# Optimization experiments

Measured on AMD Instinct MI355X. Metric: run time of the kernel, lower is better.

## Reference

```python
import jax, jax.numpy as jnp
import numpy as np

D_MODEL = 512
HEADS = 8
MAX_LEN = 2048


def setup_inputs() -> dict:
    key = jax.random.key(0)
    ks = jax.random.split(key, 8)
    b, t, e, h = 2, 2048, D_MODEL, HEADS
    s = e // h
    x = jax.random.normal(ks[0], (b, t, e), dtype=jnp.float32)
    mask = jax.random.randint(ks[1], (b, t), 0, 2).astype(jnp.int32)
    Wq = jax.random.normal(ks[2], (s, s), dtype=jnp.float32) / np.sqrt(s)
    Wk = jax.random.normal(ks[3], (s, s), dtype=jnp.float32) / np.sqrt(s)
    Wv = jax.random.normal(ks[4], (s, s), dtype=jnp.float32) / np.sqrt(s)
    Er = jax.random.normal(ks[5], (h, MAX_LEN, s), dtype=jnp.float32)
    Wo = jax.random.normal(ks[6], (e, e), dtype=jnp.float32) / np.sqrt(e)
    bo = jnp.zeros((e,), dtype=jnp.float32)
    return {"x": x, "mask": mask, "heads": h, "Wq": Wq, "Wk": Wk, "Wv": Wv,
            "Er": Er, "Wo": Wo, "bo": bo}


def reference(x, mask, heads, Wq, Wk, Wv, Er, Wo, bo):
    b, t, e = x.shape
    h = heads
    s = e // h
    x4 = x.reshape(b, t, h, s)
    # per-head shared linear projections (nn.Linear applies x @ W^T), then (b,h,t,s)
    q = jnp.einsum('bthi,oi->bhto', x4, Wq)
    k = jnp.einsum('bthi,oi->bhto', x4, Wk)
    v = jnp.einsum('bthi,oi->bhto', x4, Wv)
    # relative position scores: QEr computed on UNSCALED queries (as in source)
    Er_t = Er[:, Er.shape[1] - t:, :]                  # (h, t, s)
    qe = jnp.einsum('bhts,hls->bhtl', q, Er_t)          # (b, h, t, t)
    idx = jnp.arange(t)
    # _mask_positions: zero where col < t-1-row (flipped upper triangle)
    keep = (idx[None, :] >= (t - 1 - idx[:, None]))
    qe = jnp.where(keep[None, None], qe, 0.0)
    # _skew: pad one column on the left, reshape (t, t+1)->(t+1, t), drop first row
    padded = jnp.pad(qe, ((0, 0), (0, 0), (0, 0), (1, 0)))
    srel = padded.reshape(b, h, t + 1, t)[:, :, 1:, :]  # (b, h, t, t)
    scale = e ** (-0.25)
    scores = jnp.einsum('bhts,bhls->bhtl', q * scale, k * scale) + srel
    neg = jnp.float32(-1e9)
    causal = idx[None, :] > idx[:, None]                # future positions
    scores = jnp.where(causal[None, None], neg, scores)
    # padding mask zeroes entire query rows
    scores = jnp.where(mask[:, None, :, None] == 0, neg, scores)
    probs = jax.nn.softmax(scores, axis=-1)
    out = jnp.einsum('bhtl,bhls->bths', probs, v)       # (b, h, t, s)
    out = out.transpose(0, 2, 1, 3).reshape(b, t, e)
    return out @ Wo.T + bo
```

## Files before the change

### kernel.cpp

```cpp
#include <hip/hip_runtime.h>


#define B_ 2
#define T_ 2048
#define E_ 512
#define H_ 8
#define SCALE2 0.044194173824159216f

typedef __attribute__((ext_vector_type(8))) short bf16x8;
typedef __attribute__((ext_vector_type(4))) float f32x4;

#define MFMA(a,b,c) __builtin_amdgcn_mfma_f32_16x16x32_bf16((a),(b),(c),0,0,0)

__device__ __forceinline__ unsigned short f2bf(float f){
  unsigned u = __builtin_bit_cast(unsigned, f);
  u += 0x7fffu + ((u >> 16) & 1u);
  return (unsigned short)(u >> 16);
}
__device__ __forceinline__ float bf2f(unsigned short h){
  unsigned u = ((unsigned)h) << 16;
  return __builtin_bit_cast(float, u);
}

__global__ __launch_bounds__(256) void prep_qkv(
    const float* __restrict__ x,
    const float* __restrict__ Wq, const float* __restrict__ Wk, const float* __restrict__ Wv,
    unsigned short* __restrict__ qh, unsigned short* __restrict__ ql,
    unsigned short* __restrict__ kb, unsigned short* __restrict__ vb)
{
  int wid = blockIdx.x*4 + (threadIdx.x>>6);
  int o   = threadIdx.x & 63;
  int bh  = wid & 15;
  int rest = wid >> 4;
  int chunk = rest & 127;
  int m = rest >> 7;
  const float* W = (m==0) ? Wq : (m==1) ? Wk : Wv;
  float4 wv[16];
  #pragma unroll
  for (int j=0;j<16;++j) wv[j] = reinterpret_cast<const float4*>(W)[o*16+j];
  if (m==1){
    #pragma unroll
    for (int j=0;j<16;++j){ wv[j].x*=SCALE2; wv[j].y*=SCALE2; wv[j].z*=SCALE2; wv[j].w*=SCALE2; }
  }
  int b = bh>>3, h = bh&7;
  unsigned short* out0 = (m==0) ? qh : (m==1) ? kb : vb;
  for (int tl=0; tl<16; ++tl){
    int t = chunk*16 + tl;
    const float4* xr = reinterpret_cast<const float4*>(x + ((size_t)(b*T_ + t))*E_ + h*64);
    float a0=0.f,a1=0.f,a2=0.f,a3=0.f;
    #pragma unroll
    for (int j=0;j<16;++j){
      float4 xv = xr[j];
      a0 += xv.x*wv[j].x; a1 += xv.y*wv[j].y; a2 += xv.z*wv[j].z; a3 += xv.w*wv[j].w;
    }
    float acc = (a0+a1)+(a2+a3);
    size_t oi = ((size_t)bh*T_ + t)*64 + o;
    if (m==0){
      unsigned short hq = f2bf(acc);
      out0[oi] = hq;
      ql[oi] = f2bf(acc - bf2f(hq));
    } else {
      out0[oi] = f2bf(acc);
    }
  }
}

__global__ void prep_er(const float* __restrict__ Er,
                        unsigned short* __restrict__ eh, unsigned short* __restrict__ el)
{
  int i = (blockIdx.x*blockDim.x + threadIdx.x)*4;
  float4 v = *reinterpret_cast<const float4*>(Er + i);
  unsigned short h0=f2bf(v.x), h1=f2bf(v.y), h2=f2bf(v.z), h3=f2bf(v.w);
  *reinterpret_cast<ushort4*>(&eh[i]) = make_ushort4(h0,h1,h2,h3);
  *reinterpret_cast<ushort4*>(&el[i]) = make_ushort4(
      f2bf(v.x-bf2f(h0)), f2bf(v.y-bf2f(h1)), f2bf(v.z-bf2f(h2)), f2bf(v.w-bf2f(h3)));
}

__global__ void prep_wo(const float* __restrict__ Wo, unsigned short* __restrict__ wob){
  int i = (blockIdx.x*blockDim.x + threadIdx.x)*4;
  float4 v = *reinterpret_cast<const float4*>(Wo + i);
  *reinterpret_cast<ushort4*>(&wob[i]) = make_ushort4(f2bf(v.x),f2bf(v.y),f2bf(v.z),f2bf(v.w));
}

__global__ __launch_bounds__(256) void vsum1(const unsigned short* __restrict__ vb,
                                             float* __restrict__ vpart)
{
  __shared__ float red[4][64];
  int bh = blockIdx.x >> 3, ch = blockIdx.x & 7;
  int s = threadIdx.x & 63, sub = threadIdx.x >> 6;
  const unsigned short* p = vb + ((size_t)bh*T_ + ch*256 + sub*64)*64 + s;
  float acc = 0.f;
  #pragma unroll 8
  for (int t=0;t<64;++t) acc += bf2f(p[(size_t)t*64]);
  red[sub][s] = acc;
  __syncthreads();
  if (sub==0) vpart[(size_t)(bh*8+ch)*64 + s] = red[0][s]+red[1][s]+red[2][s]+red[3][s];
}
__global__ void vsum2(const float* __restrict__ vpart, float* __restrict__ vsum){
  int bh = blockIdx.x, s = threadIdx.x;
  float a = 0.f;
  #pragma unroll
  for (int c=0;c<8;++c) a += vpart[(size_t)(bh*8+c)*64 + s];
  vsum[bh*64+s] = a;
}

__global__ __launch_bounds__(256,2) void attn(
  const unsigned short* __restrict__ qh, const unsigned short* __restrict__ ql,
  const unsigned short* __restrict__ kb, const unsigned short* __restrict__ vb,
  const unsigned short* __restrict__ eh, const unsigned short* __restrict__ el,
  const int* __restrict__ mask, const float* __restrict__ vsum,
  unsigned short* __restrict__ ao)
{
  __shared__ float QEs[4][128][20];
  __shared__ unsigned short Ps[4][16][72];
  __shared__ unsigned short Vt[64][72];

  const int tid = threadIdx.x;
  const int w = tid >> 6, lane = tid & 63, g = lane >> 4, q15 = lane & 15;
  const int bid = blockIdx.x;
  const int bh = bid & 15;
  const int u = bid >> 4;
  const int rt = (u < 16) ? (2*u) : (63 - 2*u);
  const int i0 = rt * 64;
  const int b = bh >> 3, h = bh & 7;

  const size_t qoff = ((size_t)bh*T_ + i0 + 16*w + q15)*64 + 8*g;
  const bf16x8 qa00 = *(const bf16x8*)(qh + qoff);
  const bf16x8 qa01 = *(const bf16x8*)(qh + qoff + 32);
  const bf16x8 qa10 = *(const bf16x8*)(ql + qoff);
  const bf16x8 qa11 = *(const bf16x8*)(ql + qoff + 32);

  f32x4 oacc[4];
  float mrun[4], lrun[4];
  const f32x4 fz = {0.f,0.f,0.f,0.f};
  #pragma unroll
  for (int n=0;n<4;++n) oacc[n] = fz;
  #pragma unroll
  for (int p=0;p<4;++p){ mrun[p] = -1e30f; lrun[p] = 0.f; }

  const int ntiles = i0/64 + 1;
  const int lstart0 = (T_-64) - i0;
  for (int tI=0; tI<ntiles; ++tI){
    const int j0 = tI*64;
    const int lstart = lstart0 + j0;
    bf16x8 kf[4][2];
    #pragma unroll
    for (int n=0;n<4;++n){
      const unsigned short* kp = kb + ((size_t)bh*T_ + j0 + 16*n + q15)*64 + 8*g;
      kf[n][0] = *(const bf16x8*)kp;
      kf[n][1] = *(const bf16x8*)(kp+32);
    }
    const int key = tid & 63, sh = tid >> 6;
    bf16x8 vv0 = *(const bf16x8*)(vb + ((size_t)bh*T_ + j0 + key)*64 + 8*sh);
    bf16x8 vv1 = *(const bf16x8*)(vb + ((size_t)bh*T_ + j0 + key)*64 + 8*sh + 32);
    __syncthreads();
    #pragma unroll
    for (int jj=0;jj<8;++jj) Vt[8*sh+jj][key]    = (unsigned short)vv0[jj];
    #pragma unroll
    for (int jj=0;jj<8;++jj) Vt[8*sh+32+jj][key] = (unsigned short)vv1[jj];

    const int nhalf = (tI==0) ? 2 : 1;
    for (int half=0; half<nhalf; ++half){
      const int lb = (tI==0) ? (lstart + 64*half) : (lstart + 64);
      bf16x8 pe[4][4];
      #pragma unroll
      for (int g2=0; g2<4; ++g2){
        int ln = lb + 16*g2 + q15;
        int l = (ln > T_-1) ? (T_-1) : ln;
        const unsigned short* ep  = eh + ((size_t)h*T_ + l)*64 + 8*g;
        const unsigned short* ep2 = el + ((size_t)h*T_ + l)*64 + 8*g;
        pe[g2][0] = *(const bf16x8*)ep;
        pe[g2][1] = *(const bf16x8*)(ep+32);
        pe[g2][2] = *(const bf16x8*)ep2;
        pe[g2][3] = *(const bf16x8*)(ep2+32);
      }
      #pragma unroll
      for (int g2=0; g2<4; ++g2){
        int slot = (lb + 16*g2 + q15) & 127;
        f32x4 qe = {0.f,0.f,0.f,0.f};
        qe = MFMA(qa00, pe[g2][0], qe); qe = MFMA(qa01, pe[g2][1], qe);
        qe = MFMA(qa10, pe[g2][0], qe); qe = MFMA(qa11, pe[g2][1], qe);
        qe = MFMA(qa00, pe[g2][2], qe); qe = MFMA(qa01, pe[g2][3], qe);
        *(f32x4*)&QEs[w][slot][4*g] = qe;
      }
    }
    f32x4 sacc[4];
    #pragma unroll
    for (int n=0;n<4;++n){
      f32x4 s = fz;
      s = MFMA(qa00, kf[n][0], s); s = MFMA(qa01, kf[n][1], s);
      sacc[n] = s;
    }
    const bool lastT = (tI == ntiles-1);
    float pv[4][4];
    float tmax[4] = {-1e30f,-1e30f,-1e30f,-1e30f};
    #pragma unroll
    for (int n=0;n<4;++n){
      #pragma unroll
      for (int p=0;p<4;++p){
        int r = 16*w + 4*g + p;
        int c = 16*n + q15;
        int slot = (lstart + 63 - r + c) & 127;
        float s = sacc[n][p] + QEs[w][slot][4*g + p];
        if (lastT && c > r) s = -1e30f;
        pv[n][p] = s;
        tmax[p] = fmaxf(tmax[p], s);
      }
    }
    #pragma unroll
    for (int p=0;p<4;++p){
      float m = tmax[p];
      m = fmaxf(m, __shfl_xor(m,1)); m = fmaxf(m, __shfl_xor(m,2));
      m = fmaxf(m, __shfl_xor(m,4)); m = fmaxf(m, __shfl_xor(m,8));
      float mn = fmaxf(mrun[p], m);
      float al = __expf(mrun[p] - mn);
      mrun[p] = mn;
      lrun[p] *= al;
      oacc[0][p]*=al; oacc[1][p]*=al; oacc[2][p]*=al; oacc[3][p]*=al;
      float sum = 0.f;
      #pragma unroll
      for (int n=0;n<4;++n){
        float e = __expf(pv[n][p] - mn);
        pv[n][p] = e;
        sum += e;
      }
      sum += __shfl_xor(sum,1); sum += __shfl_xor(sum,2);
      sum += __shfl_xor(sum,4); sum += __shfl_xor(sum,8);
      lrun[p] += sum;
      #pragma unroll
      for (int n=0;n<4;++n) Ps[w][4*g+p][16*n+q15] = f2bf(pv[n][p]);
    }
    __syncthreads();
    bf16x8 pa0 = *(const bf16x8*)&Ps[w][q15][8*g];
    bf16x8 pa1 = *(const bf16x8*)&Ps[w][q15][8*g+32];
    #pragma unroll
    for (int ns=0; ns<4; ++ns){
      bf16x8 v0 = *(const bf16x8*)&Vt[16*ns+q15][8*g];
      bf16x8 v1 = *(const bf16x8*)&Vt[16*ns+q15][8*g+32];
      oacc[ns] = MFMA(pa0, v0, oacc[ns]);
      oacc[ns] = MFMA(pa1, v1, oacc[ns]);
    }
  }
  #pragma unroll
  for (int p=0;p<4;++p){
    int r = i0 + 16*w + 4*g + p;
    int mk = mask[b*T_ + r];
    float inv = 1.f / lrun[p];
    int rr = h*256 + (r >> 3);
    int cb2 = (r & 7)*64;
    #pragma unroll
    for (int n=0;n<4;++n){
      int sc = 16*n + q15;
      float val = mk ? oacc[n][p]*inv : vsum[bh*64+sc]*(1.f/2048.f);
      ao[((size_t)(b*T_ + rr))*E_ + cb2 + sc] = f2bf(val);
    }
  }
}

__global__ __launch_bounds__(256) void outproj(
  const unsigned short* __restrict__ ao, const unsigned short* __restrict__ wob,
  const float* __restrict__ bo, float* __restrict__ out)
{
  int tid = threadIdx.x;
  int w = tid>>6, lane = tid&63, g = lane>>4, q15 = lane&15;
  int nb = blockIdx.x & 7, rb = blockIdx.x >> 3;
  size_t row = (size_t)rb*64 + 16*w + q15;
  const unsigned short* ap = ao + row*E_ + 8*g;
  const f32x4 fz = {0.f,0.f,0.f,0.f};
  f32x4 acc[4];
  #pragma unroll
  for (int n=0;n<4;++n) acc[n] = fz;
  #pragma unroll 4
  for (int kk=0; kk<16; ++kk){
    bf16x8 a = *(const bf16x8*)(ap + 32*kk);
    #pragma unroll
    for (int n=0;n<4;++n){
      bf16x8 bfr = *(const bf16x8*)(wob + ((size_t)(nb*64 + 16*n + q15))*E_ + 32*kk + 8*g);
      acc[n] = MFMA(a, bfr, acc[n]);
    }
  }
  #pragma unroll
  for (int n=0;n<4;++n){
    int col = nb*64 + 16*n + q15;
    float bv = bo[col];
    #pragma unroll
    for (int p=0;p<4;++p){
      size_t rr = (size_t)rb*64 + 16*w + 4*g + p;
      out[rr*E_ + col] = acc[n][p] + bv;
    }
  }
}

extern "C" void kernel_launch(void* const* d_in, const int* in_sizes, int n_in,
                              void* d_out, int out_size, void* d_ws, size_t ws_size,
                              hipStream_t stream)
{
  int ix=-1, ier=-1, iwo=-1, ibo=-1, c4[4], nc=0;
  for (int i=0;i<n_in;++i){
    switch(in_sizes[i]){
      case 2097152: ix  = i; break;
      case 1048576: ier = i; break;
      case 262144:  iwo = i; break;
      case 512:     ibo = i; break;
      case 4096:    if (nc<4) c4[nc++] = i; break;
      default: break;
    }
  }
  if (ix<0||ier<0||iwo<0||ibo<0||nc!=4){ ix=0;c4[0]=1;c4[1]=3;c4[2]=4;c4[3]=5;ier=6;iwo=7;ibo=8; }
  const float* x  = (const float*)d_in[ix];
  const int* mask = (const int*)d_in[c4[0]];
  const float* Wq = (const float*)d_in[c4[1]];
  const float* Wk = (const float*)d_in[c4[2]];
  const float* Wv = (const float*)d_in[c4[3]];
  const float* Er = (const float*)d_in[ier];
  const float* Wo = (const float*)d_in[iwo];
  const float* bo = (const float*)d_in[ibo];
  float* out = (float*)d_out;

  char* ws = (char*)d_ws;
  unsigned short* qh  = (unsigned short*)(ws + 0);
  unsigned short* ql  = (unsigned short*)(ws + 4194304);
  unsigned short* kb  = (unsigned short*)(ws + 8388608);
  unsigned short* vb  = (unsigned short*)(ws + 12582912);
  unsigned short* eh  = (unsigned short*)(ws + 16777216);
  unsigned short* el  = (unsigned short*)(ws + 18874368);
  unsigned short* wob = (unsigned short*)(ws + 20971520);
  unsigned short* ao  = (unsigned short*)(ws + 21495808);
  float* vsum  = (float*)(ws + 25690112);
  float* vpart = (float*)(ws + 25694208);

  hipLaunchKernelGGL(prep_qkv, dim3(1536), dim3(256), 0, stream, x, Wq, Wk, Wv, qh, ql, kb, vb);
  hipLaunchKernelGGL(prep_er,  dim3(1024), dim3(256), 0, stream, Er, eh, el);
  hipLaunchKernelGGL(prep_wo,  dim3(256),  dim3(256), 0, stream, Wo, wob);
  hipLaunchKernelGGL(vsum1,    dim3(128),  dim3(256), 0, stream, vb, vpart);
  hipLaunchKernelGGL(vsum2,    dim3(16),   dim3(64),  0, stream, vpart, vsum);
  hipLaunchKernelGGL(attn,     dim3(512),  dim3(256), 0, stream, qh, ql, kb, vb, eh, el, mask, vsum, ao);
  hipLaunchKernelGGL(outproj,  dim3(512),  dim3(256), 0, stream, ao, wob, bo, out);
}
```

Baseline: 250.1 us.

## Split long causal attention rows across two blocks with flash-decoding style merge

Query row tiles 16-31 now have their key range split into two halves processed by separate blocks. Each block writes its unnormalized output, running max and sum to a partial buffer, and a new merge kernel combines them with log-sum-exp rescaling and applies the padding mask. This is meant to balance work across more blocks (768 instead of 512) and shorten the critical path. The cost is an extra kernel launch and partial-buffer traffic. Separately, prep_qkv is given twice as many blocks, each handling 8 timesteps instead of 16.

```diff
diff --git a/kernel.cpp b/kernel.cpp
--- a/kernel.cpp
+++ b/kernel.cpp
@@ -32,8 +32,8 @@
   int o   = threadIdx.x & 63;
   int bh  = wid & 15;
   int rest = wid >> 4;
-  int chunk = rest & 127;
-  int m = rest >> 7;
+  int chunk = rest & 255;
+  int m = rest >> 8;
   const float* W = (m==0) ? Wq : (m==1) ? Wk : Wv;
   float4 wv[16];
   #pragma unroll
@@ -44,8 +44,8 @@
   }
   int b = bh>>3, h = bh&7;
   unsigned short* out0 = (m==0) ? qh : (m==1) ? kb : vb;
-  for (int tl=0; tl<16; ++tl){
-    int t = chunk*16 + tl;
+  for (int tl=0; tl<8; ++tl){
+    int t = chunk*8 + tl;
     const float4* xr = reinterpret_cast<const float4*>(x + ((size_t)(b*T_ + t))*E_ + h*64);
     float a0=0.f,a1=0.f,a2=0.f,a3=0.f;
     #pragma unroll
@@ -108,8 +108,7 @@
   const unsigned short* __restrict__ qh, const unsigned short* __restrict__ ql,
   const unsigned short* __restrict__ kb, const unsigned short* __restrict__ vb,
   const unsigned short* __restrict__ eh, const unsigned short* __restrict__ el,
-  const int* __restrict__ mask, const float* __restrict__ vsum,
-  unsigned short* __restrict__ ao)
+  float* __restrict__ part)
 {
   __shared__ float QEs[4][128][20];
   __shared__ unsigned short Ps[4][16][72];
@@ -119,10 +118,19 @@
   const int w = tid >> 6, lane = tid & 63, g = lane >> 4, q15 = lane & 15;
   const int bid = blockIdx.x;
   const int bh = bid & 15;
-  const int u = bid >> 4;
-  const int rt = (u < 16) ? (2*u) : (63 - 2*u);
+  const int unit = bid >> 4;
+  int rt, ts, te, half;
+  if (unit < 16){ rt = unit; ts = 0; te = rt+1; half = 0; }
+  else {
+    int j = unit - 16;
+    rt = 16 + (j >> 1);
+    half = j & 1;
+    int nt = rt + 1;
+    int nh = (nt + 1) >> 1;
+    if (half == 0){ ts = 0; te = nh; } else { ts = nh; te = nt; }
+  }
   const int i0 = rt * 64;
-  const int b = bh >> 3, h = bh & 7;
+  const int h = bh & 7;
 
   const size_t qoff = ((size_t)bh*T_ + i0 + 16*w + q15)*64 + 8*g;
   const bf16x8 qa00 = *(const bf16x8*)(qh + qoff);
@@ -138,9 +146,8 @@
   #pragma unroll
   for (int p=0;p<4;++p){ mrun[p] = -1e30f; lrun[p] = 0.f; }
 
-  const int ntiles = i0/64 + 1;
   const int lstart0 = (T_-64) - i0;
-  for (int tI=0; tI<ntiles; ++tI){
+  for (int tI=ts; tI<te; ++tI){
     const int j0 = tI*64;
     const int lstart = lstart0 + j0;
     bf16x8 kf[4][2];
@@ -159,9 +166,9 @@
     #pragma unroll
     for (int jj=0;jj<8;++jj) Vt[8*sh+32+jj][key] = (unsigned short)vv1[jj];
 
-    const int nhalf = (tI==0) ? 2 : 1;
-    for (int half=0; half<nhalf; ++half){
-      const int lb = (tI==0) ? (lstart + 64*half) : (lstart + 64);
+    const int nhalf = (tI==ts) ? 2 : 1;
+    for (int hf=0; hf<nhalf; ++hf){
+      const int lb = (tI==ts) ? (lstart + 64*hf) : (lstart + 64);
       bf16x8 pe[4][4];
       #pragma unroll
       for (int g2=0; g2<4; ++g2){
@@ -191,7 +198,7 @@
       s = MFMA(qa00, kf[n][0], s); s = MFMA(qa01, kf[n][1], s);
       sacc[n] = s;
     }
-    const bool lastT = (tI == ntiles-1);
+    const bool lastT = (j0 == i0);
     float pv[4][4];
     float tmax[4] = {-1e30f,-1e30f,-1e30f,-1e30f};
     #pragma unroll
@@ -244,17 +251,38 @@
   #pragma unroll
   for (int p=0;p<4;++p){
     int r = i0 + 16*w + 4*g + p;
-    int mk = mask[b*T_ + r];
-    float inv = 1.f / lrun[p];
-    int rr = h*256 + (r >> 3);
-    int cb2 = (r & 7)*64;
-    #pragma unroll
-    for (int n=0;n<4;++n){
-      int sc = 16*n + q15;
-      float val = mk ? oacc[n][p]*inv : vsum[bh*64+sc]*(1.f/2048.f);
-      ao[((size_t)(b*T_ + rr))*E_ + cb2 + sc] = f2bf(val);
-    }
-  }
+    float* prow = part + (((size_t)half*16 + bh)*T_ + r)*68;
+    #pragma unroll
+    for (int n=0;n<4;++n) prow[16*n + q15] = oacc[n][p];
+    if (q15 == 0){ prow[64] = mrun[p]; prow[65] = lrun[p]; }
+  }
+}
+
+__global__ __launch_bounds__(256) void merge_k(
+  const float* __restrict__ part, const int* __restrict__ mask,
+  const float* __restrict__ vsum, unsigned short* __restrict__ ao)
+{
+  int idx = blockIdx.x*256 + threadIdx.x;
+  int c  = idx & 63;
+  int r  = (idx >> 6) & 2047;
+  int bh = idx >> 17;
+  int b = bh >> 3, h = bh & 7;
+  const float* p0 = part + (((size_t)bh)*T_ + r)*68;
+  float m0 = p0[64], l0 = p0[65], o0 = p0[c];
+  float val;
+  if (r >= 1024){
+    const float* p1 = part + (((size_t)(16 + bh))*T_ + r)*68;
+    float m1 = p1[64], l1 = p1[65], o1 = p1[c];
+    float M = fmaxf(m0, m1);
+    float a0 = __expf(m0 - M), a1 = __expf(m1 - M);
+    val = (o0*a0 + o1*a1) / (l0*a0 + l1*a1);
+  } else {
+    val = o0 / l0;
+  }
+  if (mask[b*T_ + r] == 0) val = vsum[bh*64 + c] * (1.f/2048.f);
+  int rr = h*256 + (r >> 3);
+  int cc = (r & 7)*64 + c;
+  ao[((size_t)(b*T_ + rr))*E_ + cc] = f2bf(val);
 }
 
 __global__ __launch_bounds__(256) void outproj(
@@ -328,12 +356,14 @@
   unsigned short* ao  = (unsigned short*)(ws + 21495808);
   float* vsum  = (float*)(ws + 25690112);
   float* vpart = (float*)(ws + 25694208);
-
-  hipLaunchKernelGGL(prep_qkv, dim3(1536), dim3(256), 0, stream, x, Wq, Wk, Wv, qh, ql, kb, vb);
+  float* part  = (float*)(ws + 25790464);
+
+  hipLaunchKernelGGL(prep_qkv, dim3(3072), dim3(256), 0, stream, x, Wq, Wk, Wv, qh, ql, kb, vb);
   hipLaunchKernelGGL(prep_er,  dim3(1024), dim3(256), 0, stream, Er, eh, el);
   hipLaunchKernelGGL(prep_wo,  dim3(256),  dim3(256), 0, stream, Wo, wob);
   hipLaunchKernelGGL(vsum1,    dim3(128),  dim3(256), 0, stream, vb, vpart);
   hipLaunchKernelGGL(vsum2,    dim3(16),   dim3(64),  0, stream, vpart, vsum);
-  hipLaunchKernelGGL(attn,     dim3(512),  dim3(256), 0, stream, qh, ql, kb, vb, eh, el, mask, vsum, ao);
+  hipLaunchKernelGGL(attn,     dim3(768),  dim3(256), 0, stream, qh, ql, kb, vb, eh, el, part);
+  hipLaunchKernelGGL(merge_k,  dim3(8192), dim3(256), 0, stream, part, mask, vsum, ao);
   hipLaunchKernelGGL(outproj,  dim3(512),  dim3(256), 0, stream, ao, wob, bo, out);
 }
```

Result: slower. 271.9 us (+8.7%).
